# Performance work log

Hardware: AMD Instinct MI355X
Metric: run time of the kernel (lower is better)

The kernel has to match this reference:

```python
import jax, jax.numpy as jnp
import numpy as np

DIM = 256

def setup_inputs() -> dict:
    key = jax.random.key(0)
    ks = jax.random.split(key, 7)
    x = jax.random.normal(ks[0], (4, 4096, DIM), dtype=jnp.float32)
    s = 1.0 / np.sqrt(DIM)
    Wq = jax.random.uniform(ks[1], (DIM, DIM), jnp.float32, -s, s)
    Wk = jax.random.uniform(ks[2], (DIM, DIM), jnp.float32, -s, s)
    Wv = jax.random.uniform(ks[3], (DIM, DIM), jnp.float32, -s, s)
    bq = jax.random.uniform(ks[4], (DIM,), jnp.float32, -s, s)
    bk = jax.random.uniform(ks[5], (DIM,), jnp.float32, -s, s)
    bv = jax.random.uniform(ks[6], (DIM,), jnp.float32, -s, s)
    return {"x": x, "Wq": Wq, "bq": bq, "Wk": Wk, "bk": bk, "Wv": Wv, "bv": bv}

def reference(x, Wq, bq, Wk, bk, Wv, bv):
    # torch Linear: y = x @ W.T + b
    q = jnp.einsum('bsd,ed->bse', x, Wq) + bq
    k = jnp.einsum('bsd,ed->bse', x, Wk) + bk
    v = jnp.einsum('bsd,ed->bse', x, Wv) + bv
    scale = 1.0 / jnp.sqrt(jnp.float32(x.shape[-1]))
    scores = jnp.einsum('bse,bte->bst', q, k) * scale  # [B,S,S]
    weights = jax.nn.softmax(scores, axis=-1)
    return jnp.einsum('bst,bte->bse', weights, v)
```

## Files before the change

kernel.cpp:

```cpp
#include <hip/hip_runtime.h>

#define BB 4
#define SS 4096
#define DD 256
#define NS 4
#define BS (BB*SS)
#define KT 32
#define QT 128
#define RW 32
#define NITER ((SS/NS)/KT)

typedef _Float16 f16x8 __attribute__((ext_vector_type(8)));
typedef _Float16 f16x4 __attribute__((ext_vector_type(4)));
typedef _Float16 f16x2 __attribute__((ext_vector_type(2)));
typedef float f32x4 __attribute__((ext_vector_type(4)));

union b32tof16x8 { int i[4]; f16x8 v; };

__device__ __forceinline__ void gl2lds16(const void* g, void* l) {
    __builtin_amdgcn_global_load_lds(
        (const __attribute__((address_space(1))) void*)g,
        (__attribute__((address_space(3))) void*)l, 16, 0, 0);
}

__global__ __launch_bounds__(256) void wconv_kernel(
    const float* __restrict__ Wq, const float* __restrict__ Wk,
    const float* __restrict__ Wv, _Float16* __restrict__ wh)
{
    const int p = blockIdx.y;
    const float* W = (p == 0) ? Wq : (p == 1) ? Wk : Wv;
    _Float16* dst = wh + (size_t)p * DD * DD;
    const int i = (blockIdx.x * 256 + threadIdx.x) * 4;
    const float4 v = ((const float4*)W)[i >> 2];
    f16x4 h;
    h[0] = (_Float16)v.x; h[1] = (_Float16)v.y;
    h[2] = (_Float16)v.z; h[3] = (_Float16)v.w;
    *(f16x4*)(dst + i) = h;
}

__global__ __launch_bounds__(256, 3) void proj_kernel(
    const float* __restrict__ x, const _Float16* __restrict__ wh,
    const float* __restrict__ bq, const float* __restrict__ bk,
    const float* __restrict__ bv,
    _Float16* __restrict__ qh, _Float16* __restrict__ kh,
    _Float16* __restrict__ vt)
{
    __shared__ _Float16 xs[64 * 264];

    const int tid = threadIdx.x;
    const int p   = blockIdx.y;
    const int b   = blockIdx.x >> 6;
    const int s0  = (blockIdx.x & 63) * 64;
    const float* xb = x + ((size_t)b * SS + s0) * DD;

#pragma unroll
    for (int i = 0; i < 16; ++i) {
        int f4 = i * 256 + tid;
        int row = f4 >> 6, c4 = f4 & 63;
        const float4 v = ((const float4*)(xb + (size_t)row * DD))[c4];
        f16x4 h;
        h[0] = (_Float16)v.x; h[1] = (_Float16)v.y;
        h[2] = (_Float16)v.z; h[3] = (_Float16)v.w;
        *(f16x4*)(&xs[row * 264 + c4 * 4]) = h;
    }
    __syncthreads();

    const int wv   = tid >> 6;
    const int lane = tid & 63;
    const int lo   = lane & 15;
    const int quad = lane >> 4;

    f16x8 afr[8];
#pragma unroll
    for (int ks = 0; ks < 8; ++ks)
        afr[ks] = *(const f16x8*)(&xs[(wv * 16 + lo) * 264 + ks * 32 + quad * 8]);
    __syncthreads();

    const _Float16* W  = wh + (size_t)p * DD * DD;
    const float*    bi = (p == 0) ? bq : (p == 1) ? bk : bv;
    const float     mulv = (p == 0) ? (0.0625f * 1.44269504088896340736f) : 1.0f;

    f32x4 acc[16];
#pragma unroll
    for (int nt = 0; nt < 16; ++nt) acc[nt] = (f32x4){0.f, 0.f, 0.f, 0.f};

#pragma unroll
    for (int nt = 0; nt < 16; ++nt) {
        const _Float16* wrow = W + (size_t)(nt * 16 + lo) * DD + quad * 8;
#pragma unroll
        for (int ks = 0; ks < 8; ++ks) {
            f16x8 bfr = *(const f16x8*)(wrow + ks * 32);
            acc[nt] = __builtin_amdgcn_mfma_f32_16x16x32_f16(afr[ks], bfr, acc[nt], 0, 0, 0);
        }
    }

    if (p < 2) {
        _Float16* xw = &xs[wv * 16 * 264];
#pragma unroll
        for (int nt = 0; nt < 16; ++nt) {
            const float bias = bi[nt * 16 + lo];
#pragma unroll
            for (int r = 0; r < 4; ++r)
                xw[(quad * 4 + r) * 264 + nt * 16 + lo] =
                    (_Float16)((acc[nt][r] + bias) * mulv);
        }
        _Float16* dstb = (p == 0 ? qh : kh) + ((size_t)b * SS + s0 + wv * 16) * DD;
#pragma unroll
        for (int i = 0; i < 8; ++i) {
            const int flat = i * 64 + lane;
            const int row16 = flat >> 5, g = flat & 31;
            f16x8 v = *(const f16x8*)(&xw[row16 * 264 + g * 8]);
            *(f16x8*)(dstb + (size_t)row16 * DD + g * 8) = v;
        }
    } else {
#pragma unroll
        for (int nt = 0; nt < 16; ++nt) {
            const float bias = bi[nt * 16 + lo];
            f16x4 pk;
#pragma unroll
            for (int r = 0; r < 4; ++r) pk[r] = (_Float16)(acc[nt][r] + bias);
            *(f16x4*)(vt + ((size_t)b * DD + nt * 16 + lo) * SS
                      + s0 + wv * 16 + quad * 4) = pk;
        }
    }
}

__device__ __forceinline__ void stage_kv(
    const _Float16* kb_g, const _Float16* vb_g, int t0,
    _Float16* kt, _Float16* vt_l, int wv, int lane)
{
#pragma unroll
    for (int i = 0; i < 4; ++i) {
        const int kb = wv * 4 + i;
        {
            const int r  = kb * 2 + (lane >> 5);
            const int ps = lane & 31;
            const int cg = ps ^ (r & 15);
            gl2lds16(kb_g + (size_t)(t0 + r) * DD + cg * 8, kt + kb * 512);
        }
        {
            const int r  = kb * 16 + (lane >> 2);
            const int ps = lane & 3;
            const int cg = ps ^ ((r >> 1) & 3);
            gl2lds16(vb_g + (size_t)r * SS + t0 + cg * 8, vt_l + kb * 512);
        }
    }
}

__global__ __launch_bounds__(256, 2) void attn_kernel(
    const _Float16* __restrict__ qh, const _Float16* __restrict__ kh,
    const _Float16* __restrict__ vt, _Float16* __restrict__ part,
    float* __restrict__ ml)
{
    __shared__ _Float16 kt_s[2][KT * DD];
    __shared__ _Float16 vt_s[2][DD * KT];

    const int tid  = threadIdx.x;
    const int wv   = tid >> 6;
    const int lane = tid & 63;
    const int lo   = lane & 15;
    const int quad = lane >> 4;

    const int combo = blockIdx.x & 15;
    const int qt    = blockIdx.x >> 4;
    const int b     = combo >> 2;
    const int split = combo & 3;

    const int qrow0 = qt * QT + wv * RW;
    const _Float16* qbase = qh + ((size_t)b * SS + qrow0) * DD;

    f16x8 qf[2][8];
#pragma unroll
    for (int ntq = 0; ntq < 2; ++ntq)
#pragma unroll
        for (int ks = 0; ks < 8; ++ks)
            qf[ntq][ks] = *(const f16x8*)(qbase + (size_t)(ntq * 16 + lo) * DD + ks * 32 + quad * 8);

    f32x4 acco[2][16];
#pragma unroll
    for (int ntq = 0; ntq < 2; ++ntq)
#pragma unroll
        for (int i = 0; i < 16; ++i) acco[ntq][i] = (f32x4){0.f, 0.f, 0.f, 0.f};
    float l_lane[2] = {0.f, 0.f};

    const _Float16* kbase = kh + (size_t)b * SS * DD;
    const _Float16* vbase = vt + (size_t)b * DD * SS;
    const int tbeg = split * (SS / NS);

    const int addrA = (((quad & 1) << 5) + lo) << 2;
    const int addrB = addrA + 64;

    stage_kv(kbase, vbase, tbeg, kt_s[0], vt_s[0], wv, lane);

    for (int it = 0; it < NITER; ++it) {
        const int cur = it & 1;
        __syncthreads();
        if (it + 1 < NITER)
            stage_kv(kbase, vbase, tbeg + (it + 1) * KT,
                     kt_s[cur ^ 1], vt_s[cur ^ 1], wv, lane);

        const _Float16* kt = kt_s[cur];
        const _Float16* vv = vt_s[cur];

        f32x4 st[2][2];
#pragma unroll
        for (int i = 0; i < 2; ++i)
#pragma unroll
            for (int j = 0; j < 2; ++j) st[i][j] = (f32x4){0.f, 0.f, 0.f, 0.f};
#pragma unroll
        for (int ks = 0; ks < 8; ++ks)
#pragma unroll
            for (int ntk = 0; ntk < 2; ++ntk) {
                f16x8 kfr = *(const f16x8*)(
                    &kt[(ntk * 16 + lo) * DD + ((ks * 4 + quad) ^ lo) * 8]);
                st[ntk][0] = __builtin_amdgcn_mfma_f32_16x16x32_f16(kfr, qf[0][ks], st[ntk][0], 0, 0, 0);
                st[ntk][1] = __builtin_amdgcn_mfma_f32_16x16x32_f16(kfr, qf[1][ks], st[ntk][1], 0, 0, 0);
            }

        int ipk[2][2][2];
#pragma unroll
        for (int ntk = 0; ntk < 2; ++ntk)
#pragma unroll
            for (int ntq = 0; ntq < 2; ++ntq) {
                const float p0 = exp2f(st[ntk][ntq][0]);
                const float p1 = exp2f(st[ntk][ntq][1]);
                const float p2 = exp2f(st[ntk][ntq][2]);
                const float p3 = exp2f(st[ntk][ntq][3]);
                l_lane[ntq] += (p0 + p1) + (p2 + p3);
                ipk[ntk][ntq][0] = __builtin_bit_cast(int, __builtin_amdgcn_cvt_pkrtz(p0, p1));
                ipk[ntk][ntq][1] = __builtin_bit_cast(int, __builtin_amdgcn_cvt_pkrtz(p2, p3));
            }

        f16x8 bP[2];
        const bool hi = (quad >= 2);
#pragma unroll
        for (int ntq = 0; ntq < 2; ++ntq) {
            int j01a = __builtin_amdgcn_ds_bpermute(addrA, ipk[0][ntq][0]);
            int j01b = __builtin_amdgcn_ds_bpermute(addrA, ipk[1][ntq][0]);
            int j23a = __builtin_amdgcn_ds_bpermute(addrA, ipk[0][ntq][1]);
            int j23b = __builtin_amdgcn_ds_bpermute(addrA, ipk[1][ntq][1]);
            int j45a = __builtin_amdgcn_ds_bpermute(addrB, ipk[0][ntq][0]);
            int j45b = __builtin_amdgcn_ds_bpermute(addrB, ipk[1][ntq][0]);
            int j67a = __builtin_amdgcn_ds_bpermute(addrB, ipk[0][ntq][1]);
            int j67b = __builtin_amdgcn_ds_bpermute(addrB, ipk[1][ntq][1]);
            b32tof16x8 u;
            u.i[0] = hi ? j01b : j01a;
            u.i[1] = hi ? j23b : j23a;
            u.i[2] = hi ? j45b : j45a;
            u.i[3] = hi ? j67b : j67a;
            bP[ntq] = u.v;
        }

#pragma unroll
        for (int nte = 0; nte < 16; ++nte) {
            f16x8 vfr = *(const f16x8*)(
                &vv[(nte * 16 + lo) * 32 + (quad ^ ((lo >> 1) & 3)) * 8]);
            acco[0][nte] = __builtin_amdgcn_mfma_f32_16x16x32_f16(vfr, bP[0], acco[0][nte], 0, 0, 0);
            acco[1][nte] = __builtin_amdgcn_mfma_f32_16x16x32_f16(vfr, bP[1], acco[1][nte], 0, 0, 0);
        }
    }

    const int growb = b * SS + qt * QT + wv * RW;
    _Float16* ph = part + (size_t)split * BS * DD;
#pragma unroll
    for (int ntq = 0; ntq < 2; ++ntq) {
        const int row = growb + ntq * 16 + lo;
#pragma unroll
        for (int nte = 0; nte < 16; ++nte) {
            f16x4 pk;
#pragma unroll
            for (int r = 0; r < 4; ++r) pk[r] = (_Float16)acco[ntq][nte][r];
            *(f16x4*)(ph + (size_t)row * DD + nte * 16 + quad * 4) = pk;
        }
    }
#pragma unroll
    for (int ntq = 0; ntq < 2; ++ntq) {
        float l = l_lane[ntq];
        l += __shfl_xor(l, 16, 64);
        l += __shfl_xor(l, 32, 64);
        if (quad == 0)
            ml[(size_t)split * BS + growb + ntq * 16 + lo] = l;
    }
}

__global__ __launch_bounds__(256) void combine_kernel(
    const _Float16* __restrict__ part, const float* __restrict__ ml,
    float* __restrict__ out)
{
    const int row = blockIdx.x * 4 + (threadIdx.x >> 6);
    const int e4  = threadIdx.x & 63;

    float lsum = 0.f;
#pragma unroll
    for (int i = 0; i < NS; ++i) lsum += ml[(size_t)i * BS + row];
    const float inv = 1.f / lsum;

    float o0 = 0.f, o1 = 0.f, o2 = 0.f, o3 = 0.f;
#pragma unroll
    for (int i = 0; i < NS; ++i) {
        const f16x4 pv = ((const f16x4*)(part + ((size_t)i * BS + row) * DD))[e4];
        o0 += (float)pv[0]; o1 += (float)pv[1];
        o2 += (float)pv[2]; o3 += (float)pv[3];
    }
    float4 o = {o0 * inv, o1 * inv, o2 * inv, o3 * inv};
    ((float4*)(out + (size_t)row * DD))[e4] = o;
}

extern "C" void kernel_launch(void* const* d_in, const int* in_sizes, int n_in,
                              void* d_out, int out_size, void* d_ws, size_t ws_size,
                              hipStream_t stream) {
    const float* x  = (const float*)d_in[0];
    const float* Wq = (const float*)d_in[1];
    const float* bq = (const float*)d_in[2];
    const float* Wk = (const float*)d_in[3];
    const float* bk = (const float*)d_in[4];
    const float* Wv = (const float*)d_in[5];
    const float* bv = (const float*)d_in[6];
    float* out = (float*)d_out;

    _Float16* qh = (_Float16*)d_ws;
    _Float16* kh = qh + (size_t)BS * DD;
    _Float16* vt = kh + (size_t)BS * DD;
    _Float16* wh = vt + (size_t)BS * DD;
    _Float16* part = wh + (size_t)3 * DD * DD;
    float* ml = (float*)(part + (size_t)NS * BS * DD);

    wconv_kernel<<<dim3(64, 3), dim3(256), 0, stream>>>(Wq, Wk, Wv, wh);
    proj_kernel<<<dim3(BS / 64, 3), dim3(256), 0, stream>>>(
        x, wh, bq, bk, bv, qh, kh, vt);
    attn_kernel<<<dim3((SS / QT) * 16), dim3(256), 0, stream>>>(
        qh, kh, vt, part, ml);
    combine_kernel<<<dim3(BS / 4), dim3(256), 0, stream>>>(part, ml, out);
}
```

Before: 221.5 us.

## Stage projection weights through LDS and read V fragments directly from global memory

The projection kernel now loads each 64-row chunk of the weight matrix into swizzled LDS with async global-to-LDS copies and processes it chunk by chunk, instead of every wave reading weight fragments straight from global memory. Outputs are written per chunk through a smaller LDS tile, and the occupancy hint is dropped. In the attention kernel, V is no longer double-buffered in LDS: each wave loads its V fragments directly from global memory every iteration. This halves the attention kernel's LDS use, possibly raising occupancy, but adds uncached-latency global loads inside the inner loop and more barriers in the projection kernel.

```diff
diff --git a/kernel.cpp b/kernel.cpp
--- a/kernel.cpp
+++ b/kernel.cpp
@@ -12,7 +12,6 @@
 
 typedef _Float16 f16x8 __attribute__((ext_vector_type(8)));
 typedef _Float16 f16x4 __attribute__((ext_vector_type(4)));
-typedef _Float16 f16x2 __attribute__((ext_vector_type(2)));
 typedef float f32x4 __attribute__((ext_vector_type(4)));
 
 union b32tof16x8 { int i[4]; f16x8 v; };
@@ -38,14 +37,17 @@
     *(f16x4*)(dst + i) = h;
 }
 
-__global__ __launch_bounds__(256, 3) void proj_kernel(
+__global__ __launch_bounds__(256) void proj_kernel(
     const float* __restrict__ x, const _Float16* __restrict__ wh,
     const float* __restrict__ bq, const float* __restrict__ bk,
     const float* __restrict__ bv,
     _Float16* __restrict__ qh, _Float16* __restrict__ kh,
     _Float16* __restrict__ vt)
 {
-    __shared__ _Float16 xs[64 * 264];
+    __shared__ _Float16 smem[21000];
+    _Float16* xs = smem;
+    _Float16* ws = smem;
+    _Float16* xp = smem + 16384;
 
     const int tid = threadIdx.x;
     const int p   = blockIdx.y;
@@ -74,76 +76,76 @@
 #pragma unroll
     for (int ks = 0; ks < 8; ++ks)
         afr[ks] = *(const f16x8*)(&xs[(wv * 16 + lo) * 264 + ks * 32 + quad * 8]);
-    __syncthreads();
 
     const _Float16* W  = wh + (size_t)p * DD * DD;
     const float*    bi = (p == 0) ? bq : (p == 1) ? bk : bv;
     const float     mulv = (p == 0) ? (0.0625f * 1.44269504088896340736f) : 1.0f;
 
-    f32x4 acc[16];
-#pragma unroll
-    for (int nt = 0; nt < 16; ++nt) acc[nt] = (f32x4){0.f, 0.f, 0.f, 0.f};
-
-#pragma unroll
-    for (int nt = 0; nt < 16; ++nt) {
-        const _Float16* wrow = W + (size_t)(nt * 16 + lo) * DD + quad * 8;
-#pragma unroll
-        for (int ks = 0; ks < 8; ++ks) {
-            f16x8 bfr = *(const f16x8*)(wrow + ks * 32);
-            acc[nt] = __builtin_amdgcn_mfma_f32_16x16x32_f16(afr[ks], bfr, acc[nt], 0, 0, 0);
-        }
-    }
-
-    if (p < 2) {
-        _Float16* xw = &xs[wv * 16 * 264];
-#pragma unroll
-        for (int nt = 0; nt < 16; ++nt) {
+    for (int c = 0; c < 4; ++c) {
+        __syncthreads();
+#pragma unroll
+        for (int i = 0; i < 8; ++i) {
+            const int flat = i * 256 + tid;
+            const int e  = flat >> 5;
+            const int ps = flat & 31;
+            const int cg = ps ^ (e & 15);
+            gl2lds16(W + (size_t)(c * 64 + e) * DD + cg * 8, ws + flat * 8);
+        }
+        __syncthreads();
+
+#pragma unroll
+        for (int ntl = 0; ntl < 4; ++ntl) {
+            const int nt = c * 4 + ntl;
+            f32x4 acc = {0.f, 0.f, 0.f, 0.f};
+#pragma unroll
+            for (int ks = 0; ks < 8; ++ks) {
+                const int g = (ks * 4 + quad) ^ lo;
+                f16x8 bfr = *(const f16x8*)(ws + (ntl * 16 + lo) * 256 + g * 8);
+                acc = __builtin_amdgcn_mfma_f32_16x16x32_f16(afr[ks], bfr, acc, 0, 0, 0);
+            }
             const float bias = bi[nt * 16 + lo];
-#pragma unroll
-            for (int r = 0; r < 4; ++r)
-                xw[(quad * 4 + r) * 264 + nt * 16 + lo] =
-                    (_Float16)((acc[nt][r] + bias) * mulv);
-        }
-        _Float16* dstb = (p == 0 ? qh : kh) + ((size_t)b * SS + s0 + wv * 16) * DD;
-#pragma unroll
-        for (int i = 0; i < 8; ++i) {
-            const int flat = i * 64 + lane;
-            const int row16 = flat >> 5, g = flat & 31;
-            f16x8 v = *(const f16x8*)(&xw[row16 * 264 + g * 8]);
-            *(f16x8*)(dstb + (size_t)row16 * DD + g * 8) = v;
-        }
-    } else {
-#pragma unroll
-        for (int nt = 0; nt < 16; ++nt) {
-            const float bias = bi[nt * 16 + lo];
-            f16x4 pk;
-#pragma unroll
-            for (int r = 0; r < 4; ++r) pk[r] = (_Float16)(acc[nt][r] + bias);
-            *(f16x4*)(vt + ((size_t)b * DD + nt * 16 + lo) * SS
-                      + s0 + wv * 16 + quad * 4) = pk;
-        }
-    }
-}
-
-__device__ __forceinline__ void stage_kv(
-    const _Float16* kb_g, const _Float16* vb_g, int t0,
-    _Float16* kt, _Float16* vt_l, int wv, int lane)
+            if (p < 2) {
+                _Float16* xw = xp + wv * 16 * 72;
+#pragma unroll
+                for (int r = 0; r < 4; ++r)
+                    xw[(quad * 4 + r) * 72 + ntl * 16 + lo] =
+                        (_Float16)((acc[r] + bias) * mulv);
+            } else {
+                f16x4 pk;
+#pragma unroll
+                for (int r = 0; r < 4; ++r) pk[r] = (_Float16)(acc[r] + bias);
+                *(f16x4*)(vt + ((size_t)b * DD + nt * 16 + lo) * SS
+                          + s0 + wv * 16 + quad * 4) = pk;
+            }
+        }
+
+        if (p < 2) {
+            _Float16* xw = xp + wv * 16 * 72;
+            _Float16* dstb = (p == 0 ? qh : kh)
+                + ((size_t)b * SS + s0 + wv * 16) * DD + c * 64;
+#pragma unroll
+            for (int i = 0; i < 2; ++i) {
+                const int flat = i * 64 + lane;
+                const int row = flat >> 3, g = flat & 7;
+                f16x8 v = *(const f16x8*)(xw + row * 72 + g * 8);
+                *(f16x8*)(dstb + (size_t)row * DD + g * 8) = v;
+            }
+        }
+    }
+}
+
+__device__ __forceinline__ void stage_k(
+    const _Float16* kb_g, int t0, _Float16* kt, int wv, int lane)
 {
 #pragma unroll
     for (int i = 0; i < 4; ++i) {
         const int kb = wv * 4 + i;
-        {
-            const int r  = kb * 2 + (lane >> 5);
-            const int ps = lane & 31;
-            const int cg = ps ^ (r & 15);
-            gl2lds16(kb_g + (size_t)(t0 + r) * DD + cg * 8, kt + kb * 512);
-        }
-        {
-            const int r  = kb * 16 + (lane >> 2);
-            const int ps = lane & 3;
-            const int cg = ps ^ ((r >> 1) & 3);
-            gl2lds16(vb_g + (size_t)r * SS + t0 + cg * 8, vt_l + kb * 512);
-        }
+        const int r  = kb + ((lane >> 5) ? 16 : 0);
+        const int rr = kb * 2 + (lane >> 5);
+        const int ps = lane & 31;
+        const int cg = ps ^ (rr & 15);
+        (void)r;
+        gl2lds16(kb_g + (size_t)(t0 + rr) * DD + cg * 8, kt + kb * 512);
     }
 }
 
@@ -153,7 +155,6 @@
     float* __restrict__ ml)
 {
     __shared__ _Float16 kt_s[2][KT * DD];
-    __shared__ _Float16 vt_s[2][DD * KT];
 
     const int tid  = threadIdx.x;
     const int wv   = tid >> 6;
@@ -190,17 +191,16 @@
     const int addrA = (((quad & 1) << 5) + lo) << 2;
     const int addrB = addrA + 64;
 
-    stage_kv(kbase, vbase, tbeg, kt_s[0], vt_s[0], wv, lane);
+    stage_k(kbase, tbeg, kt_s[0], wv, lane);
 
     for (int it = 0; it < NITER; ++it) {
         const int cur = it & 1;
+        const int t0  = tbeg + it * KT;
         __syncthreads();
         if (it + 1 < NITER)
-            stage_kv(kbase, vbase, tbeg + (it + 1) * KT,
-                     kt_s[cur ^ 1], vt_s[cur ^ 1], wv, lane);
+            stage_k(kbase, t0 + KT, kt_s[cur ^ 1], wv, lane);
 
         const _Float16* kt = kt_s[cur];
-        const _Float16* vv = vt_s[cur];
 
         f32x4 st[2][2];
 #pragma unroll
@@ -253,8 +253,7 @@
 
 #pragma unroll
         for (int nte = 0; nte < 16; ++nte) {
-            f16x8 vfr = *(const f16x8*)(
-                &vv[(nte * 16 + lo) * 32 + (quad ^ ((lo >> 1) & 3)) * 8]);
+            f16x8 vfr = *(const f16x8*)(vbase + (size_t)(nte * 16 + lo) * SS + t0 + quad * 8);
             acco[0][nte] = __builtin_amdgcn_mfma_f32_16x16x32_f16(vfr, bP[0], acco[0][nte], 0, 0, 0);
             acco[1][nte] = __builtin_amdgcn_mfma_f32_16x16x32_f16(vfr, bP[1], acco[1][nte], 0, 0, 0);
         }
```

Measured after the change: 278.0 us. 1.26x slower.

## Stage projection weights through double-buffered swizzled LDS chunks in proj kernel

Applied to the files above, without the earlier changes.

The projection kernel now loads W in 32-row chunks into double-buffered, XOR-swizzled shared memory using async global-to-LDS loads. Previously every wave read W fragments straight from global memory. Accumulators shrink from 16 tiles to 2 per chunk, which lowers register pressure, and the occupancy hint of 3 in launch_bounds is dropped. Output is written per chunk through a small LDS transpose buffer, which adds a barrier per chunk and narrower stores.

```diff
diff --git a/kernel.cpp b/kernel.cpp
--- a/kernel.cpp
+++ b/kernel.cpp
@@ -12,7 +12,6 @@
 
 typedef _Float16 f16x8 __attribute__((ext_vector_type(8)));
 typedef _Float16 f16x4 __attribute__((ext_vector_type(4)));
-typedef _Float16 f16x2 __attribute__((ext_vector_type(2)));
 typedef float f32x4 __attribute__((ext_vector_type(4)));
 
 union b32tof16x8 { int i[4]; f16x8 v; };
@@ -38,14 +37,16 @@
     *(f16x4*)(dst + i) = h;
 }
 
-__global__ __launch_bounds__(256, 3) void proj_kernel(
+__global__ __launch_bounds__(256) void proj_kernel(
     const float* __restrict__ x, const _Float16* __restrict__ wh,
     const float* __restrict__ bq, const float* __restrict__ bk,
     const float* __restrict__ bv,
     _Float16* __restrict__ qh, _Float16* __restrict__ kh,
     _Float16* __restrict__ vt)
 {
-    __shared__ _Float16 xs[64 * 264];
+    __shared__ _Float16 smem[19000];
+    _Float16* xs = smem;
+    _Float16* xp = smem + 16384;
 
     const int tid = threadIdx.x;
     const int p   = blockIdx.y;
@@ -80,47 +81,61 @@
     const float*    bi = (p == 0) ? bq : (p == 1) ? bk : bv;
     const float     mulv = (p == 0) ? (0.0625f * 1.44269504088896340736f) : 1.0f;
 
-    f32x4 acc[16];
-#pragma unroll
-    for (int nt = 0; nt < 16; ++nt) acc[nt] = (f32x4){0.f, 0.f, 0.f, 0.f};
-
-#pragma unroll
-    for (int nt = 0; nt < 16; ++nt) {
-        const _Float16* wrow = W + (size_t)(nt * 16 + lo) * DD + quad * 8;
+    auto stage_w = [&](int c, _Float16* ws) {
+#pragma unroll
+        for (int i = 0; i < 4; ++i) {
+            const int flat = i * 256 + tid;
+            const int e  = flat >> 5;
+            const int ps = flat & 31;
+            const int cg = ps ^ (e & 15);
+            gl2lds16(W + (size_t)(c * 32 + e) * DD + cg * 8, ws + flat * 8);
+        }
+    };
+
+    stage_w(0, smem);
+
+    for (int c = 0; c < 8; ++c) {
+        __syncthreads();
+        if (c + 1 < 8) stage_w(c + 1, smem + ((c + 1) & 1) * 8192);
+        const _Float16* ws = smem + (c & 1) * 8192;
+
+        f32x4 acc[2];
+        acc[0] = (f32x4){0.f, 0.f, 0.f, 0.f};
+        acc[1] = (f32x4){0.f, 0.f, 0.f, 0.f};
 #pragma unroll
         for (int ks = 0; ks < 8; ++ks) {
-            f16x8 bfr = *(const f16x8*)(wrow + ks * 32);
-            acc[nt] = __builtin_amdgcn_mfma_f32_16x16x32_f16(afr[ks], bfr, acc[nt], 0, 0, 0);
-        }
-    }
-
-    if (p < 2) {
-        _Float16* xw = &xs[wv * 16 * 264];
-#pragma unroll
-        for (int nt = 0; nt < 16; ++nt) {
-            const float bias = bi[nt * 16 + lo];
-#pragma unroll
-            for (int r = 0; r < 4; ++r)
-                xw[(quad * 4 + r) * 264 + nt * 16 + lo] =
-                    (_Float16)((acc[nt][r] + bias) * mulv);
-        }
-        _Float16* dstb = (p == 0 ? qh : kh) + ((size_t)b * SS + s0 + wv * 16) * DD;
-#pragma unroll
-        for (int i = 0; i < 8; ++i) {
-            const int flat = i * 64 + lane;
-            const int row16 = flat >> 5, g = flat & 31;
-            f16x8 v = *(const f16x8*)(&xw[row16 * 264 + g * 8]);
-            *(f16x8*)(dstb + (size_t)row16 * DD + g * 8) = v;
-        }
-    } else {
-#pragma unroll
-        for (int nt = 0; nt < 16; ++nt) {
-            const float bias = bi[nt * 16 + lo];
-            f16x4 pk;
-#pragma unroll
-            for (int r = 0; r < 4; ++r) pk[r] = (_Float16)(acc[nt][r] + bias);
-            *(f16x4*)(vt + ((size_t)b * DD + nt * 16 + lo) * SS
-                      + s0 + wv * 16 + quad * 4) = pk;
+            const int g = (ks * 4 + quad) ^ lo;
+            f16x8 b0 = *(const f16x8*)(ws + (lo) * 256 + g * 8);
+            f16x8 b1 = *(const f16x8*)(ws + (16 + lo) * 256 + g * 8);
+            acc[0] = __builtin_amdgcn_mfma_f32_16x16x32_f16(afr[ks], b0, acc[0], 0, 0, 0);
+            acc[1] = __builtin_amdgcn_mfma_f32_16x16x32_f16(afr[ks], b1, acc[1], 0, 0, 0);
+        }
+
+        if (p < 2) {
+            _Float16* xw = xp + wv * 640;
+#pragma unroll
+            for (int ntl = 0; ntl < 2; ++ntl) {
+                const float bias = bi[c * 32 + ntl * 16 + lo];
+#pragma unroll
+                for (int r = 0; r < 4; ++r)
+                    xw[(quad * 4 + r) * 40 + ntl * 16 + lo] =
+                        (_Float16)((acc[ntl][r] + bias) * mulv);
+            }
+            _Float16* dstb = (p == 0 ? qh : kh)
+                + ((size_t)b * SS + s0 + wv * 16) * DD + c * 32;
+            const int row = lane >> 2, g = lane & 3;
+            f16x8 v = *(const f16x8*)(xw + row * 40 + g * 8);
+            *(f16x8*)(dstb + (size_t)row * DD + g * 8) = v;
+        } else {
+#pragma unroll
+            for (int ntl = 0; ntl < 2; ++ntl) {
+                const int e = c * 32 + ntl * 16 + lo;
+                const float bias = bi[e];
+                f16x4 pk;
+#pragma unroll
+                for (int r = 0; r < 4; ++r) pk[r] = (_Float16)(acc[ntl][r] + bias);
+                *(f16x4*)(vt + ((size_t)b * DD + e) * SS + s0 + wv * 16 + quad * 4) = pk;
+            }
         }
     }
 }
```

New measurement: 188.0 us. 1.18x faster.
